# Kernel optimization log

Measured on AMD Instinct MI355X. Metric: run time of the kernel, lower is better.

## Reference

```python
import jax, jax.numpy as jnp
import numpy as np

B, T, C = 2, 2048, 1024
H = 16
D = C // H  # 64

def setup_inputs() -> dict:
    key = jax.random.key(0)
    k1, k2, k3 = jax.random.split(key, 3)
    s = 0.02
    return {
        "x": jax.random.normal(k1, (B, T, C), dtype=jnp.float32),
        "Wqkv": jax.random.normal(k2, (C, 3 * C), dtype=jnp.float32) * s,
        "bqkv": jnp.zeros((3 * C,), dtype=jnp.float32),
        "Wproj": jax.random.normal(k3, (C, C), dtype=jnp.float32) * s,
        "bproj": jnp.zeros((C,), dtype=jnp.float32),
    }

def reference(x, Wqkv, bqkv, Wproj, bproj):
    b, t, c = x.shape
    qkv = x @ Wqkv + bqkv                       # [B,T,3C]
    qkv = qkv.reshape(b, t, 3, H, D)
    q = qkv[:, :, 0].transpose(0, 2, 1, 3)      # [B,H,T,D]
    k = qkv[:, :, 1].transpose(0, 2, 1, 3)
    v = qkv[:, :, 2].transpose(0, 2, 1, 3)
    scale = 1.0 / np.sqrt(D).astype(np.float32)
    att = jnp.einsum('bhqd,bhkd->bhqk', q, k) * scale  # [B,H,T,T]
    causal = jnp.tril(jnp.ones((t, t), dtype=bool))
    att = jnp.where(causal[None, None], att, jnp.float32(-jnp.inf))
    att = jax.nn.softmax(att, axis=-1)
    y = jnp.einsum('bhqk,bhkd->bhqd', att, v)   # [B,H,T,D]
    y = y.transpose(0, 2, 1, 3).reshape(b, t, c)
    return y @ Wproj + bproj
```

## Files before the change

kernel.cpp:

```cpp
#include <hip/hip_runtime.h>

typedef __bf16 bf16x8 __attribute__((ext_vector_type(8)));
typedef float  f32x4  __attribute__((ext_vector_type(4)));
typedef float  f32x16 __attribute__((ext_vector_type(16)));
typedef unsigned int uint32x4 __attribute__((ext_vector_type(4)));

__device__ __forceinline__ short f2bf(float f) {
  union { float f; unsigned u; } v; v.f = f;
  unsigned r = v.u + 0x7fffu + ((v.u >> 16) & 1u);
  return (short)(r >> 16);
}

__device__ __forceinline__ void gl_lds16(const short* g, short* l) {
  __builtin_amdgcn_global_load_lds((const __attribute__((address_space(1))) void*)g,
                                   (__attribute__((address_space(3))) void*)l, 16, 0, 0);
}

__device__ __forceinline__ void do_transpose(const float* __restrict__ in,
                                             short* __restrict__ out,
                                             int R, int Cc, int bx, int by,
                                             short (*tile)[65]) {
  int tx = threadIdx.x & 63, ty = threadIdx.x >> 6;
  #pragma unroll
  for (int i = ty; i < 64; i += 4)
    tile[i][tx] = f2bf(in[(size_t)(by + i) * Cc + bx + tx]);
  __syncthreads();
  #pragma unroll
  for (int i = ty; i < 64; i += 4)
    out[(size_t)(bx + i) * R + by + tx] = tile[tx][i];
}

__global__ __launch_bounds__(256) void prep_kernel(const float* __restrict__ x,
                                                   short* __restrict__ x_bf,
                                                   const float* __restrict__ Wqkv,
                                                   short* __restrict__ wqkv_t,
                                                   const float* __restrict__ Wproj,
                                                   short* __restrict__ wproj_t) {
  __shared__ short tile[64][65];
  int bid = blockIdx.x;
  if (bid < 4096) {
    int i = bid * 256 + threadIdx.x;
    float4 f = reinterpret_cast<const float4*>(x)[i];
    short4 o;
    o.x = f2bf(f.x); o.y = f2bf(f.y); o.z = f2bf(f.z); o.w = f2bf(f.w);
    reinterpret_cast<short4*>(x_bf)[i] = o;
  } else if (bid < 4864) {
    int idx = bid - 4096;
    do_transpose(Wqkv, wqkv_t, 1024, 3072, (idx % 48) * 64, (idx / 48) * 64, tile);
  } else {
    int idx = bid - 4864;
    do_transpose(Wproj, wproj_t, 1024, 1024, (idx % 16) * 64, (idx / 16) * 64, tile);
  }
}


__global__ __launch_bounds__(512, 1) void gemm_qkv(const short* __restrict__ A,
                                                   const short* __restrict__ Bt,
                                                   const float* __restrict__ bias,
                                                   short* __restrict__ qo,
                                                   short* __restrict__ ko,
                                                   short* __restrict__ vt) {
  const int K = 1024;
  __shared__ short smem[65536];
  int tid = threadIdx.x;
  int x = blockIdx.x & 7, r = blockIdx.x >> 3;
  int mtile = (x * 2 + (r & 1)) * 256;
  int ntile = (r >> 1) * 256;
  int w = tid >> 6, l = tid & 63;
  int wr = w >> 2, wc = w & 3;
  int lr = l & 15, lg = l >> 4;

  f32x4 zero4 = {0.f, 0.f, 0.f, 0.f};
  f32x4 acc[8][4];
  #pragma unroll
  for (int i = 0; i < 8; ++i)
    #pragma unroll
    for (int j = 0; j < 4; ++j) acc[i][j] = zero4;

#define STAGE_QKV(BUF, K0) do {                                                      \
    short* Ab_ = smem + (BUF) * 32768;                                               \
    short* Bb_ = Ab_ + 16384;                                                        \
    _Pragma("unroll")                                                                \
    for (int c = 0; c < 4; ++c) {                                                    \
      int idx = tid + c * 512;                                                       \
      int row = idx >> 3, kc = (idx & 7) ^ (row & 7);       \
      gl_lds16(&A[(size_t)(mtile + row) * K + (K0) + kc * 8], &Ab_[idx * 8]);        \
      gl_lds16(&Bt[(size_t)(ntile + row) * K + (K0) + kc * 8], &Bb_[idx * 8]);       \
    }                                                                                \
  } while (0)

  STAGE_QKV(0, 0);
  __syncthreads();
  int cur = 0;
  for (int it = 0; it < 16; ++it) {
    if (it < 15) STAGE_QKV(cur ^ 1, (it + 1) * 64);
    const short* Ab = smem + cur * 32768;
    const short* Bb = Ab + 16384;
    __builtin_amdgcn_s_setprio(1);
    #pragma unroll
    for (int kk = 0; kk < 2; ++kk) {
      bf16x8 af[8], bfr[4];
      #pragma unroll
      for (int i = 0; i < 8; ++i) {
        int rA = wr * 128 + i * 16 + lr;
        af[i] = *reinterpret_cast<const bf16x8*>(&Ab[rA * 64 + (((kk * 4 + lg) ^ (rA & 7)) * 8)]);
      }
      #pragma unroll
      for (int j = 0; j < 4; ++j) {
        int rB = wc * 64 + j * 16 + lr;
        bfr[j] = *reinterpret_cast<const bf16x8*>(&Bb[rB * 64 + (((kk * 4 + lg) ^ (rB & 7)) * 8)]);
      }
      #pragma unroll
      for (int i = 0; i < 8; ++i)
        #pragma unroll
        for (int j = 0; j < 4; ++j)
          acc[i][j] = __builtin_amdgcn_mfma_f32_16x16x32_bf16(af[i], bfr[j], acc[i][j], 0, 0, 0);
    }
    __builtin_amdgcn_s_setprio(0);
    __syncthreads();
    cur ^= 1;
  }
#undef STAGE_QKV

  const int sec = ntile >> 10;
  if (sec == 2) {
    #pragma unroll
    for (int j = 0; j < 4; ++j) {
      int nl = wc * 64 + j * 16 + lr;
      int d  = nl & 63;
      float bv = bias[ntile + nl];
      #pragma unroll
      for (int i = 0; i < 8; ++i) {
        int lt0 = wr * 128 + i * 16 + lg * 4;
        int c2 = (nl >> 6) * 8 + (lt0 >> 5);
        int pos = (((lt0 >> 3) & 1) << 10) + (d & 31) * 32 +
                  ((((lt0 >> 4) & 1) + ((d >> 5) << 1)) << 3) + (lt0 & 7);
        short4 pk;
        pk.x = f2bf(acc[i][j][0] + bv);
        pk.y = f2bf(acc[i][j][1] + bv);
        pk.z = f2bf(acc[i][j][2] + bv);
        pk.w = f2bf(acc[i][j][3] + bv);
        *reinterpret_cast<short4*>(&smem[c2 * 2048 + pos]) = pk;
      }
    }
  } else {
    const float sc = (sec == 0) ? 0.18033688f : 1.0f;
    #pragma unroll
    for (int j = 0; j < 4; ++j) {
      int nl = wc * 64 + j * 16 + lr;
      int d  = nl & 63;
      float bv = bias[ntile + nl];
      int dpart = (((d >> 3) & 1) << 10) + ((d >> 4) << 3) + (d & 7);
      #pragma unroll
      for (int i = 0; i < 8; ++i) {
        #pragma unroll
        for (int r2 = 0; r2 < 4; ++r2) {
          int lt = wr * 128 + i * 16 + lg * 4 + r2;
          int c2 = (nl >> 6) * 8 + (lt >> 5);
          smem[c2 * 2048 + (lt & 31) * 32 + dpart] = f2bf((acc[i][j][r2] + bv) * sc);
        }
      }
    }
  }
  __syncthreads();
  short* dst = (sec == 0) ? qo : ((sec == 1) ? ko : vt);
  int bb  = mtile >> 11;
  int h0  = (ntile & 1023) >> 6;
  int gt0 = (mtile & 2047) >> 5;
  #pragma unroll
  for (int c2 = 0; c2 < 32; ++c2) {
    size_t base = (size_t)(bb * 16 + h0 + (c2 >> 3)) * 131072 +
                  (size_t)(gt0 + (c2 & 7)) * 2048;
    *reinterpret_cast<uint2*>(&dst[base + tid * 4]) =
        *reinterpret_cast<const uint2*>(&smem[c2 * 2048 + tid * 4]);
  }
}

template<int DIAG>
__device__ __forceinline__ void attn_step(const short* __restrict__ kp,
                                          const short* __restrict__ vp,
                                          const bf16x8* qf,
                                          f32x16& y0, f32x16& y1,
                                          float& m, float& li,
                                          int lq, int hl) {
  f32x16 s;
  #pragma unroll
  for (int r = 0; r < 16; ++r) s[r] = -m;
  __builtin_amdgcn_s_setprio(1);
  #pragma unroll
  for (int ks = 0; ks < 4; ++ks) {
    bf16x8 kf = *reinterpret_cast<const bf16x8*>(kp + ks * 8);
    s = __builtin_amdgcn_mfma_f32_32x32x16_bf16(kf, qf[ks], s, 0, 0, 0);
  }
  __builtin_amdgcn_s_setprio(0);
  if (DIAG) {
    #pragma unroll
    for (int r = 0; r < 16; ++r) {
      int kvl = (r & 3) + 8 * (r >> 2) + 4 * hl;
      if (kvl > lq) s[r] = -1e30f;
    }
  }
  float t0 = fmaxf(fmaxf(s[0], s[1]), s[2]);
  float t1 = fmaxf(fmaxf(s[3], s[4]), s[5]);
  float t2 = fmaxf(fmaxf(s[6], s[7]), s[8]);
  float t3 = fmaxf(fmaxf(s[9], s[10]), s[11]);
  float t4 = fmaxf(fmaxf(s[12], s[13]), s[14]);
  float pm = fmaxf(fmaxf(fmaxf(t0, t1), t2), fmaxf(fmaxf(t3, t4), s[15]));
  if (!__all(pm <= 8.0f)) {
    float pmu = fmaxf(pm, __shfl_xor(pm, 32));
    float delta = fmaxf(pmu, 0.0f);
    float sc = __builtin_amdgcn_exp2f(-delta);
    m += delta;
    li *= sc;
    #pragma unroll
    for (int r = 0; r < 16; ++r) { y0[r] *= sc; y1[r] *= sc; s[r] -= delta; }
  }
  unsigned u[8];
  float rs = 0.f;
  #pragma unroll
  for (int rq = 0; rq < 4; ++rq) {
    float p0 = __builtin_amdgcn_exp2f(s[4 * rq + 0]);
    float p1 = __builtin_amdgcn_exp2f(s[4 * rq + 1]);
    float p2 = __builtin_amdgcn_exp2f(s[4 * rq + 2]);
    float p3 = __builtin_amdgcn_exp2f(s[4 * rq + 3]);
    rs += (p0 + p1) + (p2 + p3);
    asm("v_cvt_pk_bf16_f32 %0, %1, %2" : "=v"(u[rq * 2 + 0]) : "v"(p0), "v"(p1));
    asm("v_cvt_pk_bf16_f32 %0, %1, %2" : "=v"(u[rq * 2 + 1]) : "v"(p2), "v"(p3));
  }
  li += rs;
  asm volatile("v_permlane32_swap_b32 %0, %1" : "+v"(u[0]), "+v"(u[2]));
  asm volatile("v_permlane32_swap_b32 %0, %1" : "+v"(u[1]), "+v"(u[3]));
  asm volatile("v_permlane32_swap_b32 %0, %1" : "+v"(u[4]), "+v"(u[6]));
  asm volatile("v_permlane32_swap_b32 %0, %1" : "+v"(u[5]), "+v"(u[7]));
  uint32x4 w0 = {u[0], u[1], u[2], u[3]};
  uint32x4 w1 = {u[4], u[5], u[6], u[7]};
  bf16x8 pa0 = __builtin_bit_cast(bf16x8, w0);
  bf16x8 pa1 = __builtin_bit_cast(bf16x8, w1);
  __builtin_amdgcn_s_setprio(1);
  {
    bf16x8 vf00 = *reinterpret_cast<const bf16x8*>(vp);
    bf16x8 vf01 = *reinterpret_cast<const bf16x8*>(vp + 8);
    bf16x8 vf10 = *reinterpret_cast<const bf16x8*>(vp + 16);
    bf16x8 vf11 = *reinterpret_cast<const bf16x8*>(vp + 24);
    y0 = __builtin_amdgcn_mfma_f32_32x32x16_bf16(vf00, pa0, y0, 0, 0, 0);
    y0 = __builtin_amdgcn_mfma_f32_32x32x16_bf16(vf01, pa1, y0, 0, 0, 0);
    y1 = __builtin_amdgcn_mfma_f32_32x32x16_bf16(vf10, pa0, y1, 0, 0, 0);
    y1 = __builtin_amdgcn_mfma_f32_32x32x16_bf16(vf11, pa1, y1, 0, 0, 0);
  }
  __builtin_amdgcn_s_setprio(0);
}

__global__ __launch_bounds__(256, 4) void attn_kernel(const short* __restrict__ q,
                                                      const short* __restrict__ k,
                                                      const short* __restrict__ vt,
                                                      short* __restrict__ y) {
  __shared__ float partL[3][4][64][4];
  __shared__ float stm[4][32], stl[4][32];
  const int bid = blockIdx.x;
  const int p = bid >> 5;
  const int b5 = bid & 31;
  const int bh = (b5 & 7) * 4 + (b5 >> 3);
  const int tid = threadIdx.x;
  const int w = tid >> 6;
  const int l = tid & 63;
  const int lq = l & 31, hl = l >> 5;
  const short* qb = q + (size_t)bh * 131072;
  const short* kb = k + (size_t)bh * 131072;
  const short* vb = vt + (size_t)bh * 131072;
  const int b_ = bh >> 4, h_ = bh & 15;

  #pragma unroll 1
  for (int half = 0; half < 2; ++half) {
    const int t = half ? p : (63 - p);

    bf16x8 qf[4];
    {
      const short* qp = qb + (size_t)t * 2048 + l * 32;
      #pragma unroll
      for (int ks = 0; ks < 4; ++ks)
        qf[ks] = *reinterpret_cast<const bf16x8*>(qp + ks * 8);
    }

    f32x16 y0, y1;
    #pragma unroll
    for (int r = 0; r < 16; ++r) { y0[r] = 0.f; y1[r] = 0.f; }
    float m = 0.f, li = 0.f;

    const short* kp = kb + (size_t)w * 2048 + l * 32;
    const short* vp = vb + (size_t)w * 2048 + l * 32;
    for (int it = w; it < t; it += 4) {
      attn_step<0>(kp, vp, qf, y0, y1, m, li, lq, hl);
      kp += 4 * 2048;
      vp += 4 * 2048;
    }
    if ((t & 3) == w) {
      const short* kpd = kb + (size_t)t * 2048 + l * 32;
      const short* vpd = vb + (size_t)t * 2048 + l * 32;
      attn_step<1>(kpd, vpd, qf, y0, y1, m, li, lq, hl);
    }
    li += __shfl_xor(li, 32);

    if (hl == 0) { stm[w][lq] = m; stl[w][lq] = li; }
    __syncthreads();
    float m0 = stm[0][lq], m1 = stm[1][lq], m2 = stm[2][lq], m3 = stm[3][lq];
    float M = fmaxf(fmaxf(m0, m1), fmaxf(m2, m3));
    float L = stl[0][lq] * __builtin_amdgcn_exp2f(m0 - M) +
              stl[1][lq] * __builtin_amdgcn_exp2f(m1 - M) +
              stl[2][lq] * __builtin_amdgcn_exp2f(m2 - M) +
              stl[3][lq] * __builtin_amdgcn_exp2f(m3 - M);
    float sc = __builtin_amdgcn_exp2f(m - M);
    #pragma unroll
    for (int r = 0; r < 16; ++r) { y0[r] *= sc; y1[r] *= sc; }

    if (w > 0) {
      #pragma unroll
      for (int c = 0; c < 4; ++c) {
        f32x4 v0s = {y0[4 * c + 0], y0[4 * c + 1], y0[4 * c + 2], y0[4 * c + 3]};
        *reinterpret_cast<f32x4*>(&partL[w - 1][c][l][0]) = v0s;
      }
    }
    __syncthreads();
    if (w == 0) {
      #pragma unroll
      for (int o = 0; o < 3; ++o)
        #pragma unroll
        for (int c = 0; c < 4; ++c) {
          f32x4 v0s = *reinterpret_cast<const f32x4*>(&partL[o][c][l][0]);
          #pragma unroll
          for (int r = 0; r < 4; ++r) y0[4 * c + r] += v0s[r];
        }
    }
    __syncthreads();
    if (w > 0) {
      #pragma unroll
      for (int c = 0; c < 4; ++c) {
        f32x4 v1s = {y1[4 * c + 0], y1[4 * c + 1], y1[4 * c + 2], y1[4 * c + 3]};
        *reinterpret_cast<f32x4*>(&partL[w - 1][c][l][0]) = v1s;
      }
    }
    __syncthreads();
    if (w == 0) {
      #pragma unroll
      for (int o = 0; o < 3; ++o)
        #pragma unroll
        for (int c = 0; c < 4; ++c) {
          f32x4 v1s = *reinterpret_cast<const f32x4*>(&partL[o][c][l][0]);
          #pragma unroll
          for (int r = 0; r < 4; ++r) y1[4 * c + r] += v1s[r];
        }
      float inv = 1.0f / L;
      short* yrow = &y[(size_t)(b_ * 2048 + 32 * t + lq) * 1024 + h_ * 64];
      #pragma unroll
      for (int dt = 0; dt < 2; ++dt) {
        const f32x16& yy = dt ? y1 : y0;
        #pragma unroll
        for (int rq = 0; rq < 4; ++rq) {
          int d0 = dt * 32 + 8 * rq + 4 * hl;
          uint2 pk;
          pk.x = (unsigned)(unsigned short)f2bf(yy[4 * rq + 0] * inv) |
                 ((unsigned)(unsigned short)f2bf(yy[4 * rq + 1] * inv) << 16);
          pk.y = (unsigned)(unsigned short)f2bf(yy[4 * rq + 2] * inv) |
                 ((unsigned)(unsigned short)f2bf(yy[4 * rq + 3] * inv) << 16);
          *reinterpret_cast<uint2*>(yrow + d0) = pk;
        }
      }
    }
    __syncthreads();
  }
}

__global__ __launch_bounds__(256, 3) void gemm_proj(const short* __restrict__ A,
                                                    const short* __restrict__ Bt,
                                                    const float* __restrict__ bias,
                                                    float* __restrict__ out) {
  const int K = 1024;
  __shared__ short smem[24576];
  int tid = threadIdx.x;
  int x = blockIdx.x & 7, r = blockIdx.x >> 3;
  int ntile = (x * 2 + (r & 1)) * 64, mtile = (r >> 1) * 128;
  int w = tid >> 6, l = tid & 63;
  int lr = l & 15, lg = l >> 4;

  f32x4 zero4 = {0.f, 0.f, 0.f, 0.f};
  f32x4 acc[2][4];
  #pragma unroll
  for (int i = 0; i < 2; ++i)
    #pragma unroll
    for (int j = 0; j < 4; ++j) acc[i][j] = zero4;

#define STAGE_PRJ(BUF, K0) do {                                                      \
    short* Ab_ = smem + (BUF) * 12288;                                               \
    short* Bb_ = Ab_ + 8192;                                                         \
    _Pragma("unroll")                                                                \
    for (int c = 0; c < 4; ++c) {                                                    \
      int idx = tid + c * 256;                                                       \
      int row = idx >> 3, kc = (idx & 7) ^ (row & 7);                                \
      gl_lds16(&A[(size_t)(mtile + row) * K + (K0) + kc * 8], &Ab_[idx * 8]);        \
    }                                                                                \
    _Pragma("unroll")                                                                \
    for (int c = 0; c < 2; ++c) {                                                    \
      int idx = tid + c * 256;                                                       \
      int row = idx >> 3, kc = (idx & 7) ^ (row & 7);                                \
      gl_lds16(&Bt[(size_t)(ntile + row) * K + (K0) + kc * 8], &Bb_[idx * 8]);       \
    }                                                                                \
  } while (0)

  STAGE_PRJ(0, 0);
  __syncthreads();
  int cur = 0;
  for (int it = 0; it < 16; ++it) {
    if (it < 15) STAGE_PRJ(cur ^ 1, (it + 1) * 64);
    const short* Ab = smem + cur * 12288;
    const short* Bb = Ab + 8192;
    __builtin_amdgcn_s_setprio(1);
    #pragma unroll
    for (int kk = 0; kk < 2; ++kk) {
      bf16x8 af[2], bfr[4];
      #pragma unroll
      for (int i = 0; i < 2; ++i) {
        int rA = w * 32 + i * 16 + lr;
        af[i] = *reinterpret_cast<const bf16x8*>(&Ab[rA * 64 + (((kk * 4 + lg) ^ (rA & 7)) * 8)]);
      }
      #pragma unroll
      for (int j = 0; j < 4; ++j) {
        int rB = j * 16 + lr;
        bfr[j] = *reinterpret_cast<const bf16x8*>(&Bb[rB * 64 + (((kk * 4 + lg) ^ (rB & 7)) * 8)]);
      }
      #pragma unroll
      for (int i = 0; i < 2; ++i)
        #pragma unroll
        for (int j = 0; j < 4; ++j)
          acc[i][j] = __builtin_amdgcn_mfma_f32_16x16x32_bf16(af[i], bfr[j], acc[i][j], 0, 0, 0);
    }
    __builtin_amdgcn_s_setprio(0);
    __syncthreads();
    cur ^= 1;
  }
#undef STAGE_PRJ

  #pragma unroll
  for (int j = 0; j < 4; ++j) {
    int n = ntile + j * 16 + lr;
    float bv = bias[n];
    #pragma unroll
    for (int i = 0; i < 2; ++i) {
      #pragma unroll
      for (int r2 = 0; r2 < 4; ++r2) {
        int m = mtile + w * 32 + i * 16 + lg * 4 + r2;
        out[(size_t)m * 1024 + n] = acc[i][j][r2] + bv;
      }
    }
  }
}

extern "C" void kernel_launch(void* const* d_in, const int* in_sizes, int n_in,
                              void* d_out, int out_size, void* d_ws, size_t ws_size,
                              hipStream_t stream) {
  const float* x     = (const float*)d_in[0];
  const float* Wqkv  = (const float*)d_in[1];
  const float* bqkv  = (const float*)d_in[2];
  const float* Wproj = (const float*)d_in[3];
  const float* bproj = (const float*)d_in[4];
  float* out = (float*)d_out;

  const size_t M4 = 4096ull * 1024ull;
  short* ws = (short*)d_ws;
  short* x_bf    = ws;
  short* wqkv_t  = ws + M4;
  short* wproj_t = ws + M4 + 3ull * 1024 * 1024;
  short* qb      = wproj_t + 1024ull * 1024;
  short* kb      = qb + M4;
  short* vtb     = kb + M4;
  short* yb      = x_bf;

  prep_kernel<<<5120, 256, 0, stream>>>(x, x_bf, Wqkv, wqkv_t, Wproj, wproj_t);
  gemm_qkv<<<192, 512, 0, stream>>>(x_bf, wqkv_t, bqkv, qb, kb, vtb);
  attn_kernel<<<1024, 256, 0, stream>>>(qb, kb, vtb, yb);
  gemm_proj<<<512, 256, 0, stream>>>(yb, wproj_t, bproj, out);
}
```

Before: 101.9 us.

## Process two KV tiles per iteration with independent softmax accumulators

Each wave now handles two key/value tiles per loop iteration, keeping two separate online-softmax states (max, sum and output accumulators) and merging them after the loop. The two QK^T MFMA chains are interleaved so the independent work can hide MFMA latency and the serial dependency on the running max. The cost is higher register pressure from a second set of 32-float accumulators, which under launch_bounds(256,4) could cause spills or lower occupancy.

```diff
diff --git a/kernel.cpp b/kernel.cpp
--- a/kernel.cpp
+++ b/kernel.cpp
@@ -177,22 +177,11 @@
 }
 
 template<int DIAG>
-__device__ __forceinline__ void attn_step(const short* __restrict__ kp,
+__device__ __forceinline__ void attn_tail(f32x16& s,
                                           const short* __restrict__ vp,
-                                          const bf16x8* qf,
                                           f32x16& y0, f32x16& y1,
                                           float& m, float& li,
                                           int lq, int hl) {
-  f32x16 s;
-  #pragma unroll
-  for (int r = 0; r < 16; ++r) s[r] = -m;
-  __builtin_amdgcn_s_setprio(1);
-  #pragma unroll
-  for (int ks = 0; ks < 4; ++ks) {
-    bf16x8 kf = *reinterpret_cast<const bf16x8*>(kp + ks * 8);
-    s = __builtin_amdgcn_mfma_f32_32x32x16_bf16(kf, qf[ks], s, 0, 0, 0);
-  }
-  __builtin_amdgcn_s_setprio(0);
   if (DIAG) {
     #pragma unroll
     for (int r = 0; r < 16; ++r) {
@@ -250,6 +239,50 @@
   __builtin_amdgcn_s_setprio(0);
 }
 
+template<int DIAG>
+__device__ __forceinline__ void attn_step(const short* __restrict__ kp,
+                                          const short* __restrict__ vp,
+                                          const bf16x8* qf,
+                                          f32x16& y0, f32x16& y1,
+                                          float& m, float& li,
+                                          int lq, int hl) {
+  f32x16 s;
+  #pragma unroll
+  for (int r = 0; r < 16; ++r) s[r] = -m;
+  __builtin_amdgcn_s_setprio(1);
+  #pragma unroll
+  for (int ks = 0; ks < 4; ++ks) {
+    bf16x8 kf = *reinterpret_cast<const bf16x8*>(kp + ks * 8);
+    s = __builtin_amdgcn_mfma_f32_32x32x16_bf16(kf, qf[ks], s, 0, 0, 0);
+  }
+  __builtin_amdgcn_s_setprio(0);
+  attn_tail<DIAG>(s, vp, y0, y1, m, li, lq, hl);
+}
+
+__device__ __forceinline__ void attn_step2(const short* __restrict__ kpA,
+                                           const short* __restrict__ vpA,
+                                           const short* __restrict__ kpB,
+                                           const short* __restrict__ vpB,
+                                           const bf16x8* qf,
+                                           f32x16& yA0, f32x16& yA1, float& mA, float& liA,
+                                           f32x16& yB0, f32x16& yB1, float& mB, float& liB,
+                                           int lq, int hl) {
+  f32x16 sA, sB;
+  #pragma unroll
+  for (int r = 0; r < 16; ++r) { sA[r] = -mA; sB[r] = -mB; }
+  __builtin_amdgcn_s_setprio(1);
+  #pragma unroll
+  for (int ks = 0; ks < 4; ++ks) {
+    bf16x8 kfA = *reinterpret_cast<const bf16x8*>(kpA + ks * 8);
+    sA = __builtin_amdgcn_mfma_f32_32x32x16_bf16(kfA, qf[ks], sA, 0, 0, 0);
+    bf16x8 kfB = *reinterpret_cast<const bf16x8*>(kpB + ks * 8);
+    sB = __builtin_amdgcn_mfma_f32_32x32x16_bf16(kfB, qf[ks], sB, 0, 0, 0);
+  }
+  __builtin_amdgcn_s_setprio(0);
+  attn_tail<0>(sA, vpA, yA0, yA1, mA, liA, lq, hl);
+  attn_tail<0>(sB, vpB, yB0, yB1, mB, liB, lq, hl);
+}
+
 __global__ __launch_bounds__(256, 4) void attn_kernel(const short* __restrict__ q,
                                                       const short* __restrict__ k,
                                                       const short* __restrict__ vt,
@@ -281,22 +314,36 @@
         qf[ks] = *reinterpret_cast<const bf16x8*>(qp + ks * 8);
     }
 
-    f32x16 y0, y1;
-    #pragma unroll
-    for (int r = 0; r < 16; ++r) { y0[r] = 0.f; y1[r] = 0.f; }
-    float m = 0.f, li = 0.f;
+    f32x16 yA0, yA1, yB0, yB1;
+    #pragma unroll
+    for (int r = 0; r < 16; ++r) { yA0[r] = 0.f; yA1[r] = 0.f; yB0[r] = 0.f; yB1[r] = 0.f; }
+    float mA = 0.f, liA = 0.f, mB = 0.f, liB = 0.f;
 
     const short* kp = kb + (size_t)w * 2048 + l * 32;
     const short* vp = vb + (size_t)w * 2048 + l * 32;
-    for (int it = w; it < t; it += 4) {
-      attn_step<0>(kp, vp, qf, y0, y1, m, li, lq, hl);
-      kp += 4 * 2048;
-      vp += 4 * 2048;
-    }
-    if ((t & 3) == w) {
-      const short* kpd = kb + (size_t)t * 2048 + l * 32;
-      const short* vpd = vb + (size_t)t * 2048 + l * 32;
-      attn_step<1>(kpd, vpd, qf, y0, y1, m, li, lq, hl);
+    int it = w;
+    for (; it + 4 < t; it += 8) {
+      attn_step2(kp, vp, kp + 4 * 2048, vp + 4 * 2048, qf,
+                 yA0, yA1, mA, liA, yB0, yB1, mB, liB, lq, hl);
+      kp += 8 * 2048;
+      vp += 8 * 2048;
+    }
+    if (it < t)
+      attn_step<0>(kp, vp, qf, yA0, yA1, mA, liA, lq, hl);
+    if ((t & 3) == w)
+      attn_step<1>(kb + (size_t)t * 2048 + l * 32, vb + (size_t)t * 2048 + l * 32,
+                   qf, yA0, yA1, mA, liA, lq, hl);
+
+    float M2 = fmaxf(mA, mB);
+    float eA = __builtin_amdgcn_exp2f(mA - M2);
+    float eB = __builtin_amdgcn_exp2f(mB - M2);
+    float m = M2;
+    float li = liA * eA + liB * eB;
+    f32x16 y0, y1;
+    #pragma unroll
+    for (int r = 0; r < 16; ++r) {
+      y0[r] = yA0[r] * eA + yB0[r] * eB;
+      y1[r] = yA1[r] * eA + yB1[r] * eB;
     }
     li += __shfl_xor(li, 32);
 
```

Measured after the change: 151.0 us. 48.2% more time.
